# Kernel optimization log

Hardware: AMD Instinct MI355X
Metric: run time of the kernel (lower is better)

The kernel has to match this reference:

```python
import jax, jax.numpy as jnp
import numpy as np

N = 100000; E = 1600000; D_IN = 128; HID = 64; HEADS = 2; OUT = 2; B = 8192
NEG_SLOPE = 0.2


def gat_conv(x, edge_index, W, a_src, a_dst, bias):
    """PyG-style GATConv with add_self_loops=True, concat=False (mean over heads).
    x: [N, Fin], W: [Fin, H*C], a_src/a_dst: [H, C], bias: [C]."""
    n = x.shape[0]
    H, C = a_src.shape
    h = (x @ W).reshape(n, H, C)                      # [N,H,C]
    s_src = (h * a_src[None]).sum(-1)                 # [N,H]
    s_dst = (h * a_dst[None]).sum(-1)                 # [N,H]
    loop = jnp.arange(n, dtype=edge_index.dtype)
    src = jnp.concatenate([edge_index[0], loop])      # [E+N]
    dst = jnp.concatenate([edge_index[1], loop])
    e = jax.nn.leaky_relu(s_src[src] + s_dst[dst], NEG_SLOPE)   # [E+N,H]
    # segment softmax over edges grouped by destination node
    m = jax.ops.segment_max(e, dst, num_segments=n)             # [N,H]
    ex = jnp.exp(e - m[dst])
    z = jax.ops.segment_sum(ex, dst, num_segments=n)            # [N,H]
    alpha = ex / z[dst]                                          # [E+N,H]
    msg = h[src] * alpha[:, :, None]                             # [E+N,H,C]
    out = jax.ops.segment_sum(msg, dst, num_segments=n)         # [N,H,C]
    return out.mean(axis=1) + bias                               # concat=False -> mean over heads


def setup_inputs() -> dict:
    key = jax.random.key(0)
    ks = jax.random.split(key, 32)
    def p(k, shape, fan_in):
        return (jax.random.normal(k, shape, dtype=jnp.float32) / np.sqrt(fan_in)).astype(jnp.float32)
    inp = {}
    inp["x_l"] = jax.random.normal(ks[0], (N, D_IN), dtype=jnp.float32)
    inp["x_r"] = jax.random.normal(ks[1], (N, D_IN), dtype=jnp.float32)
    inp["edge_index_l"] = jax.random.randint(ks[2], (2, E), 0, N, dtype=jnp.int64 if jax.config.jax_enable_x64 else jnp.int32)
    inp["edge_index_r"] = jax.random.randint(ks[3], (2, E), 0, N, dtype=jnp.int64 if jax.config.jax_enable_x64 else jnp.int32)
    inp["labels_l"] = jax.random.randint(ks[4], (B,), 0, N)
    inp["labels_r"] = jax.random.randint(ks[5], (B,), 0, N)
    i = 6
    for side in ("l", "r"):
        inp[f"w1{side}"] = p(ks[i], (D_IN, HEADS * HID), D_IN); i += 1
        inp[f"as1{side}"] = p(ks[i], (HEADS, HID), HID); i += 1
        inp[f"ad1{side}"] = p(ks[i], (HEADS, HID), HID); i += 1
        inp[f"b1{side}"] = jnp.zeros((HID,), jnp.float32)
        inp[f"w2{side}"] = p(ks[i], (HID, HEADS * HID), HID); i += 1
        inp[f"as2{side}"] = p(ks[i], (HEADS, HID), HID); i += 1
        inp[f"ad2{side}"] = p(ks[i], (HEADS, HID), HID); i += 1
        inp[f"b2{side}"] = jnp.zeros((HID,), jnp.float32)
    inp["fc1_w"] = p(ks[i], (2 * HID, HID), 2 * HID); i += 1
    inp["fc1_b"] = jnp.zeros((HID,), jnp.float32)
    inp["fc2_w"] = p(ks[i], (HID, OUT), HID); i += 1
    inp["fc2_b"] = jnp.zeros((OUT,), jnp.float32)
    return inp


def reference(x_l, x_r, edge_index_l, edge_index_r, labels_l, labels_r,
              w1l, as1l, ad1l, b1l, w2l, as2l, ad2l, b2l,
              w1r, as1r, ad1r, b1r, w2r, as2r, ad2r, b2r,
              fc1_w, fc1_b, fc2_w, fc2_b):
    # left tower (dropout is identity in eval mode)
    hl = jax.nn.relu(gat_conv(x_l, edge_index_l, w1l, as1l, ad1l, b1l))
    hl = jax.nn.relu(gat_conv(hl, edge_index_l, w2l, as2l, ad2l, b2l))
    # right tower
    hr = jax.nn.relu(gat_conv(x_r, edge_index_r, w1r, as1r, ad1r, b1r))
    hr = jax.nn.relu(gat_conv(hr, edge_index_r, w2r, as2r, ad2r, b2r))
    # merge_graphs: gather node features per labeled pair, concat
    merged = jnp.concatenate([hl[labels_l], hr[labels_r]], axis=-1)  # [B, 2*HID]
    x = jax.nn.relu(merged @ fc1_w + fc1_b)
    return x @ fc2_w + fc2_b
```

## Files before the change

### kernel.cpp

```cpp
#include <hip/hip_runtime.h>
#include <hip/hip_bf16.h>
#include <hip/hip_fp16.h>

constexpr int NN   = 100000;
constexpr int EE   = 1600000;
constexpr int BB   = 8192;
constexpr int PAD  = 48;
constexpr float NEG_SLOPE = 0.2f;

constexpr int GBM = 128;
constexpr int GB = (NN + GBM - 1) / GBM;
constexpr int AB2 = NN / 8;

constexpr int BSPAN = 256;
constexpr int NB    = (NN + BSPAN - 1) / BSPAN;
constexpr int BCAP  = 5120;
constexpr int CHA   = 4096;
constexpr int NCH   = (EE + CHA - 1) / CHA;

typedef _Float16 f16x8 __attribute__((ext_vector_type(8)));
typedef _Float16 f16x4 __attribute__((ext_vector_type(4)));
typedef float    f32x4 __attribute__((ext_vector_type(4)));

__device__ __forceinline__ float4 ld4(const float* p) { return *(const float4*)p; }

template <typename TIN, int K>
__device__ __forceinline__
void gemm_mfma_body(int bid, const TIN* __restrict__ x,
                    const __half* __restrict__ Wimg,
                    const float* __restrict__ a_src, const float* __restrict__ a_dst,
                    __half* __restrict__ h,
                    float* __restrict__ ssrc, float* __restrict__ sdst,
                    char* lds) {
    constexpr bool HAS_LO = sizeof(TIN) == 4;
    char* const xh = lds;
    char* const xl = HAS_LO ? (lds + 16384) : lds;
    char* const wh = lds + (HAS_LO ? 32768 : 16384);
    char* const wl = wh + 16384;

    const int tid = threadIdx.x;
    const int wid = tid >> 6;
    const int lane = tid & 63;
    const int l15 = lane & 15;
    const int lg = lane >> 4;
    const int row0 = bid * GBM;

    f32x4 acc[2][8];
    #pragma unroll
    for (int i = 0; i < 2; ++i)
        #pragma unroll
        for (int j = 0; j < 8; ++j) acc[i][j] = (f32x4)0.f;

    for (int kt = 0; kt < K; kt += 64) {
        __syncthreads();
        if constexpr (HAS_LO) {
            #pragma unroll
            for (int i = 0; i < 8; ++i) {
                int idx = tid + i * 256;
                int row = idx >> 4, c4 = idx & 15;
                int grow = row0 + row; if (grow >= NN) grow = NN - 1;
                float4 v = ld4(&x[(size_t)grow * K + kt + c4 * 4]);
                f16x4 hv, lv;
                float f0 = v.x; _Float16 h0 = (_Float16)f0; hv[0] = h0; lv[0] = (_Float16)(f0 - (float)h0);
                float f1 = v.y; _Float16 h1 = (_Float16)f1; hv[1] = h1; lv[1] = (_Float16)(f1 - (float)h1);
                float f2 = v.z; _Float16 h2 = (_Float16)f2; hv[2] = h2; lv[2] = (_Float16)(f2 - (float)h2);
                float f3 = v.w; _Float16 h3 = (_Float16)f3; hv[3] = h3; lv[3] = (_Float16)(f3 - (float)h3);
                int byt = row * 128 + ((c4 * 8) ^ ((row & 7) << 4));
                *(f16x4*)(xh + byt) = hv;
                *(f16x4*)(xl + byt) = lv;
            }
        } else {
            #pragma unroll
            for (int i = 0; i < 4; ++i) {
                int idx = tid + i * 256;
                int row = idx >> 3, c8 = idx & 7;
                int grow = row0 + row; if (grow >= NN) grow = NN - 1;
                uint4 v = *(const uint4*)&x[(size_t)grow * 64 + c8 * 8];
                int byt = row * 128 + ((c8 * 16) ^ ((row & 7) << 4));
                *(uint4*)(xh + byt) = v;
            }
        }
        {
            const uint4* ws = (const uint4*)((const char*)Wimg + (size_t)(kt >> 6) * 32768);
            uint4* wd = (uint4*)wh;
            #pragma unroll
            for (int i = 0; i < 8; ++i) wd[tid + i * 256] = ws[tid + i * 256];
        }
        __syncthreads();

        #pragma unroll
        for (int ks = 0; ks < 2; ++ks) {
            const int koff = ks * 64 + lg * 16;
            f16x8 ah[2], al[2];
            #pragma unroll
            for (int rt = 0; rt < 2; ++rt) {
                int row = wid * 32 + rt * 16 + l15;
                int byt = row * 128 + (koff ^ ((row & 7) << 4));
                ah[rt] = *(const f16x8*)(xh + byt);
                if constexpr (HAS_LO) al[rt] = *(const f16x8*)(xl + byt);
            }
            #pragma unroll
            for (int ct = 0; ct < 8; ++ct) {
                int col = ct * 16 + l15;
                int byt = col * 128 + (koff ^ ((col & 7) << 4));
                f16x8 bh = *(const f16x8*)(wh + byt);
                f16x8 bl = *(const f16x8*)(wl + byt);
                #pragma unroll
                for (int rt = 0; rt < 2; ++rt) {
                    acc[rt][ct] = __builtin_amdgcn_mfma_f32_16x16x32_f16(ah[rt], bh, acc[rt][ct], 0, 0, 0);
                    acc[rt][ct] = __builtin_amdgcn_mfma_f32_16x16x32_f16(ah[rt], bl, acc[rt][ct], 0, 0, 0);
                    if constexpr (HAS_LO)
                        acc[rt][ct] = __builtin_amdgcn_mfma_f32_16x16x32_f16(al[rt], bh, acc[rt][ct], 0, 0, 0);
                }
            }
        }
    }

    float sv[8], dv[8];
    #pragma unroll
    for (int ct = 0; ct < 8; ++ct) {
        sv[ct] = a_src[ct * 16 + l15];
        dv[ct] = a_dst[ct * 16 + l15];
    }
    #pragma unroll
    for (int rt = 0; rt < 2; ++rt) {
        #pragma unroll
        for (int r = 0; r < 4; ++r) {
            int row = row0 + wid * 32 + rt * 16 + lg * 4 + r;
            bool ok = row < NN;
            if (ok) {
                #pragma unroll
                for (int ct = 0; ct < 8; ++ct)
                    h[(size_t)row * 128 + ct * 16 + l15] = __float2half(acc[rt][ct][r]);
            }
            float ps0 = 0.f, pd0 = 0.f, ps1 = 0.f, pd1 = 0.f;
            #pragma unroll
            for (int ct = 0; ct < 4; ++ct) {
                ps0 = fmaf(acc[rt][ct][r], sv[ct], ps0);
                pd0 = fmaf(acc[rt][ct][r], dv[ct], pd0);
                ps1 = fmaf(acc[rt][ct + 4][r], sv[ct + 4], ps1);
                pd1 = fmaf(acc[rt][ct + 4][r], dv[ct + 4], pd1);
            }
            ps0 += __shfl_xor(ps0, 1); pd0 += __shfl_xor(pd0, 1);
            ps1 += __shfl_xor(ps1, 1); pd1 += __shfl_xor(pd1, 1);
            ps0 += __shfl_xor(ps0, 2); pd0 += __shfl_xor(pd0, 2);
            ps1 += __shfl_xor(ps1, 2); pd1 += __shfl_xor(pd1, 2);
            ps0 += __shfl_xor(ps0, 4); pd0 += __shfl_xor(pd0, 4);
            ps1 += __shfl_xor(ps1, 4); pd1 += __shfl_xor(pd1, 4);
            ps0 += __shfl_xor(ps0, 8); pd0 += __shfl_xor(pd0, 8);
            ps1 += __shfl_xor(ps1, 8); pd1 += __shfl_xor(pd1, 8);
            if (ok && l15 == 0) {
                ssrc[row * 2 + 0] = ps0;
                ssrc[row * 2 + 1] = ps1;
                sdst[row * 2 + 0] = pd0;
                sdst[row * 2 + 1] = pd1;
            }
        }
    }
}

__global__ __launch_bounds__(256)
void k_bucket(const int* __restrict__ el, const int* __restrict__ er,
              int* __restrict__ buf, int* __restrict__ gcur,
              const float* __restrict__ w1l, const float* __restrict__ w1r,
              const float* __restrict__ w2l, const float* __restrict__ w2r,
              __half* __restrict__ wi1l, __half* __restrict__ wi1r,
              __half* __restrict__ wi2l, __half* __restrict__ wi2r) {
    const int blk0 = blockIdx.x;
    if (blk0 >= 2 * NCH) {
        const int id = blk0 - 2 * NCH;
        const float* W;
        __half* img;
        int kt;
        if (id < 4) {
            W = (id >> 1) ? w1r : w1l;
            img = ((id >> 1) ? wi1r : wi1l) + (size_t)(id & 1) * 16384;
            kt = (id & 1) * 64;
        } else {
            W = (id == 5) ? w2r : w2l;
            img = (id == 5) ? wi2r : wi2l;
            kt = 0;
        }
        _Float16* imgh = (_Float16*)img;
        _Float16* imgl = imgh + 8192;
        for (int i = threadIdx.x; i < 8192; i += 256) {
            int kk = i >> 7, col = i & 127;
            float f = W[(size_t)(kt + kk) * 128 + col];
            _Float16 hi = (_Float16)f;
            _Float16 lo = (_Float16)(f - (float)hi);
            int hidx = col * 64 + (kk ^ ((col & 7) << 3));
            imgh[hidx] = hi;
            imgl[hidx] = lo;
        }
        return;
    }

    __shared__ int2 P0[CHA];
    __shared__ int2 P1[CHA];
    __shared__ int hist[NB];
    __shared__ int st[NB];
    __shared__ int ofs[NB];
    __shared__ int base[NB];
    __shared__ int sc[512];

    const int blk = blk0;
    const bool right = blk >= NCH;
    const int* __restrict__ e = right ? er : el;
    const int sideoff = right ? NB : 0;
    const int cbase = (right ? blk - NCH : blk) * CHA;
    int cnum = EE - cbase; if (cnum > CHA) cnum = CHA;
    const int t = threadIdx.x;

    for (int i = t; i < cnum; i += 256) {
        int2 p; p.x = e[EE + cbase + i]; p.y = e[cbase + i];
        P0[i] = p;
    }
    for (int i = t; i < NB; i += 256) hist[i] = 0;
    __syncthreads();
    for (int i = t; i < cnum; i += 256) atomicAdd(&hist[P0[i].x >> 8], 1);
    __syncthreads();

    sc[t]       = (t < NB)       ? hist[t]       : 0;
    sc[t + 256] = (t + 256 < NB) ? hist[t + 256] : 0;
    __syncthreads();
    for (int off = 1; off < 512; off <<= 1) {
        int a0 = sc[t];
        int a1 = sc[t + 256];
        int b0 = (t >= off)       ? sc[t - off]       : 0;
        int b1 = (t + 256 >= off) ? sc[t + 256 - off] : 0;
        __syncthreads();
        sc[t] = a0 + b0;
        sc[t + 256] = a1 + b1;
        __syncthreads();
    }
    for (int i = t; i < NB; i += 256) {
        int s = sc[i] - hist[i];
        st[i] = s;
        ofs[i] = s;
    }
    __syncthreads();
    for (int i = t; i < cnum; i += 256) {
        int2 p = P0[i];
        int pos = atomicAdd(&ofs[p.x >> 8], 1);
        P1[pos] = p;
    }
    __syncthreads();
    for (int i = t; i < NB; i += 256)
        base[i] = hist[i] ? atomicAdd(&gcur[sideoff + i], hist[i]) : 0;
    __syncthreads();
    for (int j = t; j < cnum; j += 256) {
        int2 p = P1[j];
        int bk = p.x >> 8;
        buf[(size_t)(sideoff + bk) * BCAP + base[bk] + (j - st[bk])] =
            (p.y << 8) | (p.x & 255);
    }
}

__device__ __forceinline__
void csr_body(int blk, const int* __restrict__ buf, const int* __restrict__ gcur,
              int* __restrict__ cntl, int* __restrict__ cntr,
              int* __restrict__ csrl, int* __restrict__ csrr, char* smem) {
    int* lcnt = (int*)smem;
    int* lcsr = (int*)(smem + 1024);

    const bool right = blk >= NB;
    const int bk = right ? blk - NB : blk;
    int* __restrict__ cnt = right ? cntr : cntl;
    int* __restrict__ csr = right ? csrr : csrl;
    const int* __restrict__ src = buf + (size_t)blk * BCAP;
    const int count = gcur[blk];
    const int lo = bk * BSPAN;
    int nn = NN - lo; if (nn > BSPAN) nn = BSPAN;
    const int t = threadIdx.x;

    for (int i = t; i < nn; i += 256) lcnt[i] = 0;
    __syncthreads();
    for (int i = t; i < count; i += 256) {
        int v = src[i];
        int ld = v & 255;
        int s  = (int)((unsigned)v >> 8);
        int slot = atomicAdd(&lcnt[ld], 1);
        lcsr[ld * PAD + slot] = s;
    }
    __syncthreads();
    const int tot4 = (nn * PAD) >> 2;
    int4* __restrict__ dst4 = (int4*)&csr[(size_t)lo * PAD];
    const int4* __restrict__ s4 = (const int4*)lcsr;
    for (int i = t; i < tot4; i += 256) dst4[i] = s4[i];
    for (int i = t; i < nn; i += 256) cnt[lo + i] = lcnt[i];
}

__global__ __launch_bounds__(256)
void k_csr_gemm1(const int* __restrict__ buf, const int* __restrict__ gcur,
                 int* __restrict__ cnt_l, int* __restrict__ cnt_r,
                 int* __restrict__ csr_l, int* __restrict__ csr_r,
                 const float* __restrict__ x_l, const float* __restrict__ x_r,
                 const __half* __restrict__ wi1l, const float* __restrict__ as1l,
                 const float* __restrict__ ad1l,
                 const __half* __restrict__ wi1r, const float* __restrict__ as1r,
                 const float* __restrict__ ad1r,
                 __half* __restrict__ h_l, __half* __restrict__ h_r,
                 float* __restrict__ ssrc_l, float* __restrict__ sdst_l,
                 float* __restrict__ ssrc_r, float* __restrict__ sdst_r) {
    __shared__ __align__(16) char smem[65536];
    int b = blockIdx.x;
    if (b < 2 * NB) {
        csr_body(b, buf, gcur, cnt_l, cnt_r, csr_l, csr_r, smem);
    } else {
        b -= 2 * NB;
        if (b < GB)
            gemm_mfma_body<float, 128>(b, x_l, wi1l, as1l, ad1l,
                                       h_l, ssrc_l, sdst_l, smem);
        else
            gemm_mfma_body<float, 128>(b - GB, x_r, wi1r, as1r, ad1r,
                                       h_r, ssrc_r, sdst_r, smem);
    }
}

__global__ __launch_bounds__(256)
void k_gemm2x(const __half* __restrict__ f_l, const __half* __restrict__ f_r,
              const __half* __restrict__ wi2l, const float* __restrict__ as2l,
              const float* __restrict__ ad2l,
              const __half* __restrict__ wi2r, const float* __restrict__ as2r,
              const float* __restrict__ ad2r,
              __half* __restrict__ h_l, __half* __restrict__ h_r,
              float* __restrict__ ssrc_l, float* __restrict__ sdst_l,
              float* __restrict__ ssrc_r, float* __restrict__ sdst_r) {
    __shared__ __align__(16) char smem[49152];
    int b = blockIdx.x;
    if (b < GB)
        gemm_mfma_body<__half, 64>(b, (const __half*)f_l, wi2l, as2l, ad2l,
                                   h_l, ssrc_l, sdst_l, smem);
    else
        gemm_mfma_body<__half, 64>(b - GB, (const __half*)f_r, wi2r, as2r, ad2r,
                                   h_r, ssrc_r, sdst_r, smem);
}

__device__ __forceinline__
void att_body(int n, const __half* __restrict__ h,
              const float* __restrict__ ssrc, const float* __restrict__ sdst,
              const int* __restrict__ cnt, const int* __restrict__ csr,
              const float* __restrict__ bias, __half* __restrict__ out) {
    const int g  = threadIdx.x & 31;
    const int hs = g >> 4;
    const int j  = g & 15;
    const int ch = g * 4;

    float sd = sdst[n * 2 + hs];
    float es = ssrc[n * 2 + hs] + sd;
    es = es > 0.f ? es : NEG_SLOPE * es;
    const float wself = __expf(es);
    float zl = 0.f;

    uint2 sv = *(const uint2*)&h[(size_t)n * 128 + ch];
    __half2 sh0 = *(__half2*)&sv.x, sh1 = *(__half2*)&sv.y;
    float2 p01 = __half22float2(sh0), p23 = __half22float2(sh1);
    float a0 = wself * p01.x, a1 = wself * p01.y;
    float a2 = wself * p23.x, a3 = wself * p23.y;

    int b = n * PAD;
    const int e = b + cnt[n];
    while (b < e) {
        int c = e - b; if (c > 16) c = 16;
        int idx = b + (j < c ? j : c - 1);
        int sj = csr[idx];
        float ev = ssrc[sj * 2 + hs] + sd;
        ev = ev > 0.f ? ev : NEG_SLOPE * ev;
        float w = (j < c) ? __expf(ev) : 0.f;
        zl += w;
        int jj = 0;
        for (; jj + 4 <= c; jj += 4) {
            int s0 = __shfl(sj, jj,     32);
            int s1 = __shfl(sj, jj + 1, 32);
            int s2 = __shfl(sj, jj + 2, 32);
            int s3 = __shfl(sj, jj + 3, 32);
            float w0 = __shfl(w, hs * 16 + jj,     32);
            float w1 = __shfl(w, hs * 16 + jj + 1, 32);
            float w2 = __shfl(w, hs * 16 + jj + 2, 32);
            float w3 = __shfl(w, hs * 16 + jj + 3, 32);
            uint2 u0 = *(const uint2*)&h[(size_t)(unsigned)(s0 * 128 + ch)];
            uint2 u1 = *(const uint2*)&h[(size_t)(unsigned)(s1 * 128 + ch)];
            uint2 u2 = *(const uint2*)&h[(size_t)(unsigned)(s2 * 128 + ch)];
            uint2 u3 = *(const uint2*)&h[(size_t)(unsigned)(s3 * 128 + ch)];
            float2 f0a = __half22float2(*(__half2*)&u0.x), f0b = __half22float2(*(__half2*)&u0.y);
            float2 f1a = __half22float2(*(__half2*)&u1.x), f1b = __half22float2(*(__half2*)&u1.y);
            float2 f2a = __half22float2(*(__half2*)&u2.x), f2b = __half22float2(*(__half2*)&u2.y);
            float2 f3a = __half22float2(*(__half2*)&u3.x), f3b = __half22float2(*(__half2*)&u3.y);
            a0 = fmaf(w0, f0a.x, a0); a1 = fmaf(w0, f0a.y, a1);
            a2 = fmaf(w0, f0b.x, a2); a3 = fmaf(w0, f0b.y, a3);
            a0 = fmaf(w1, f1a.x, a0); a1 = fmaf(w1, f1a.y, a1);
            a2 = fmaf(w1, f1b.x, a2); a3 = fmaf(w1, f1b.y, a3);
            a0 = fmaf(w2, f2a.x, a0); a1 = fmaf(w2, f2a.y, a1);
            a2 = fmaf(w2, f2b.x, a2); a3 = fmaf(w2, f2b.y, a3);
            a0 = fmaf(w3, f3a.x, a0); a1 = fmaf(w3, f3a.y, a1);
            a2 = fmaf(w3, f3b.x, a2); a3 = fmaf(w3, f3b.y, a3);
        }
        for (; jj < c; ++jj) {
            int s0   = __shfl(sj, jj, 32);
            float w0 = __shfl(w, hs * 16 + jj, 32);
            uint2 u0 = *(const uint2*)&h[(size_t)(unsigned)(s0 * 128 + ch)];
            float2 f0a = __half22float2(*(__half2*)&u0.x), f0b = __half22float2(*(__half2*)&u0.y);
            a0 = fmaf(w0, f0a.x, a0); a1 = fmaf(w0, f0a.y, a1);
            a2 = fmaf(w0, f0b.x, a2); a3 = fmaf(w0, f0b.y, a3);
        }
        b += c;
    }

    zl += __shfl_xor(zl, 1, 32);
    zl += __shfl_xor(zl, 2, 32);
    zl += __shfl_xor(zl, 4, 32);
    zl += __shfl_xor(zl, 8, 32);
    const float z = wself + zl;

    float zi = 1.f / z;
    a0 *= zi; a1 *= zi; a2 *= zi; a3 *= zi;
    a0 = 0.5f * (a0 + __shfl_xor(a0, 16));
    a1 = 0.5f * (a1 + __shfl_xor(a1, 16));
    a2 = 0.5f * (a2 + __shfl_xor(a2, 16));
    a3 = 0.5f * (a3 + __shfl_xor(a3, 16));
    if (hs == 0) {
        float4 bv = *(const float4*)&bias[ch];
        a0 += bv.x; a1 += bv.y; a2 += bv.z; a3 += bv.w;
        a0 = a0 > 0.f ? a0 : 0.f;
        a1 = a1 > 0.f ? a1 : 0.f;
        a2 = a2 > 0.f ? a2 : 0.f;
        a3 = a3 > 0.f ? a3 : 0.f;
        __align__(8) __half2 hp[2];
        hp[0] = __floats2half2_rn(a0, a1);
        hp[1] = __floats2half2_rn(a2, a3);
        *(uint2*)&out[(size_t)n * 64 + ch] = *(uint2*)hp;
    }
}

__global__ __launch_bounds__(256)
void k_att2x(const __half* __restrict__ h_l, const __half* __restrict__ h_r,
             const float* __restrict__ ssrc_l, const float* __restrict__ sdst_l,
             const float* __restrict__ ssrc_r, const float* __restrict__ sdst_r,
             const int* __restrict__ cnt_l, const int* __restrict__ csr_l,
             const int* __restrict__ cnt_r, const int* __restrict__ csr_r,
             const float* __restrict__ bias_l, const float* __restrict__ bias_r,
             __half* __restrict__ feat_l, __half* __restrict__ feat_r) {
    int blk = blockIdx.x;
    bool right = blk >= AB2;
    int n = (blk - (right ? AB2 : 0)) * 8 + (threadIdx.x >> 5);
    if (!right) att_body(n, h_l, ssrc_l, sdst_l, cnt_l, csr_l, bias_l, feat_l);
    else        att_body(n, h_r, ssrc_r, sdst_r, cnt_r, csr_r, bias_r, feat_r);
}

__global__ __launch_bounds__(256)
void k_fc(const __half* __restrict__ fl, const __half* __restrict__ fr,
          const int* __restrict__ ll, const int* __restrict__ lr,
          const float* __restrict__ w1, const float* __restrict__ b1,
          const float* __restrict__ w2, const float* __restrict__ b2,
          float* __restrict__ out) {
    int b = blockIdx.x * 4 + (threadIdx.x >> 6);
    int j = threadIdx.x & 63;
    int la = ll[b], lb = lr[b];
    float v0 = __half2float(fl[(size_t)la * 64 + j]);
    float v1 = __half2float(fr[(size_t)lb * 64 + j]);
    float acc = b1[j];
    #pragma unroll 8
    for (int k = 0; k < 64; ++k)
        acc += __shfl(v0, k, 64) * w1[k * 64 + j];
    #pragma unroll 8
    for (int k = 0; k < 64; ++k)
        acc += __shfl(v1, k, 64) * w1[(64 + k) * 64 + j];
    float x1 = acc > 0.f ? acc : 0.f;
    float p0 = x1 * w2[j * 2 + 0];
    float p1 = x1 * w2[j * 2 + 1];
    #pragma unroll
    for (int o = 32; o >= 1; o >>= 1) {
        p0 += __shfl_xor(p0, o, 64);
        p1 += __shfl_xor(p1, o, 64);
    }
    if (j == 0) {
        out[b * 2 + 0] = p0 + b2[0];
        out[b * 2 + 1] = p1 + b2[1];
    }
}

extern "C" void kernel_launch(void* const* d_in, const int* in_sizes, int n_in,
                              void* d_out, int out_size, void* d_ws, size_t ws_size,
                              hipStream_t stream) {
    const float* x_l  = (const float*)d_in[0];
    const float* x_r  = (const float*)d_in[1];
    const int* ei_l  = (const int*)d_in[2];
    const int* ei_r  = (const int*)d_in[3];
    const int* lab_l = (const int*)d_in[4];
    const int* lab_r = (const int*)d_in[5];
    const float* w1l  = (const float*)d_in[6];
    const float* as1l = (const float*)d_in[7];
    const float* ad1l = (const float*)d_in[8];
    const float* b1l  = (const float*)d_in[9];
    const float* w2l  = (const float*)d_in[10];
    const float* as2l = (const float*)d_in[11];
    const float* ad2l = (const float*)d_in[12];
    const float* b2l  = (const float*)d_in[13];
    const float* w1r  = (const float*)d_in[14];
    const float* as1r = (const float*)d_in[15];
    const float* ad1r = (const float*)d_in[16];
    const float* b1r  = (const float*)d_in[17];
    const float* w2r  = (const float*)d_in[18];
    const float* as2r = (const float*)d_in[19];
    const float* ad2r = (const float*)d_in[20];
    const float* b2r  = (const float*)d_in[21];
    const float* fc1w = (const float*)d_in[22];
    const float* fc1b = (const float*)d_in[23];
    const float* fc2w = (const float*)d_in[24];
    const float* fc2b = (const float*)d_in[25];

    char* p = (char*)d_ws;
    auto alloc = [&](size_t bytes) -> void* {
        void* q = (void*)p;
        p += (bytes + 255) & ~(size_t)255;
        return q;
    };
    __half* h_l    = (__half*)alloc((size_t)NN * 128 * 2);
    __half* h_r    = (__half*)alloc((size_t)NN * 128 * 2);
    __half* feat_l = (__half*)alloc((size_t)NN * 64 * 2);
    __half* feat_r = (__half*)alloc((size_t)NN * 64 * 2);
    float* ssrc_l = (float*)alloc((size_t)NN * 2 * 4);
    float* sdst_l = (float*)alloc((size_t)NN * 2 * 4);
    float* ssrc_r = (float*)alloc((size_t)NN * 2 * 4);
    float* sdst_r = (float*)alloc((size_t)NN * 2 * 4);
    int* cnt2  = (int*)alloc(((size_t)2 * NN + 2 * NB) * 4);
    int* csr_l = (int*)alloc((size_t)NN * PAD * 4);
    int* csr_r = (int*)alloc((size_t)NN * PAD * 4);
    __half* wi1l = (__half*)alloc(65536);
    __half* wi1r = (__half*)alloc(65536);
    __half* wi2l = (__half*)alloc(32768);
    __half* wi2r = (__half*)alloc(32768);
    int* cnt_l = cnt2;
    int* cnt_r = cnt2 + NN;
    int* gcur  = cnt2 + 2 * NN;

    int* buf = (int*)feat_l;

    hipMemsetAsync(gcur, 0, (size_t)2 * NB * 4, stream);

    k_bucket<<<2 * NCH + 6, 256, 0, stream>>>(ei_l, ei_r, buf, gcur,
                                              w1l, w1r, w2l, w2r,
                                              wi1l, wi1r, wi2l, wi2r);

    k_csr_gemm1<<<2 * NB + 2 * GB, 256, 0, stream>>>(
        buf, gcur, cnt_l, cnt_r, csr_l, csr_r,
        x_l, x_r, wi1l, as1l, ad1l, wi1r, as1r, ad1r,
        h_l, h_r, ssrc_l, sdst_l, ssrc_r, sdst_r);

    k_att2x<<<2 * AB2, 256, 0, stream>>>(h_l, h_r, ssrc_l, sdst_l, ssrc_r, sdst_r,
                                         cnt_l, csr_l, cnt_r, csr_r,
                                         b1l, b1r, feat_l, feat_r);

    k_gemm2x<<<2 * GB, 256, 0, stream>>>(feat_l, feat_r,
                                         wi2l, as2l, ad2l, wi2r, as2r, ad2r,
                                         h_l, h_r, ssrc_l, sdst_l, ssrc_r, sdst_r);

    k_att2x<<<2 * AB2, 256, 0, stream>>>(h_l, h_r, ssrc_l, sdst_l, ssrc_r, sdst_r,
                                         cnt_l, csr_l, cnt_r, csr_r,
                                         b2l, b2r, feat_l, feat_r);

    k_fc<<<(BB + 3) / 4, 256, 0, stream>>>(feat_l, feat_r, lab_l, lab_r,
                                           fc1w, fc1b, fc2w, fc2b,
                                           (float*)d_out);
}
```

Baseline: 558.1 us.

## Halve GEMM K-tile and bucket chunk to shrink LDS footprint

```diff
diff --git a/kernel.cpp b/kernel.cpp
--- a/kernel.cpp
+++ b/kernel.cpp
@@ -15,7 +15,7 @@
 constexpr int BSPAN = 256;
 constexpr int NB    = (NN + BSPAN - 1) / BSPAN;
 constexpr int BCAP  = 5120;
-constexpr int CHA   = 4096;
+constexpr int CHA   = 2048;
 constexpr int NCH   = (EE + CHA - 1) / CHA;
 
 typedef _Float16 f16x8 __attribute__((ext_vector_type(8)));
@@ -34,9 +34,9 @@
                     char* lds) {
     constexpr bool HAS_LO = sizeof(TIN) == 4;
     char* const xh = lds;
-    char* const xl = HAS_LO ? (lds + 16384) : lds;
-    char* const wh = lds + (HAS_LO ? 32768 : 16384);
-    char* const wl = wh + 16384;
+    char* const xl = HAS_LO ? (lds + 8192) : lds;
+    char* const wh = lds + (HAS_LO ? 16384 : 8192);
+    char* const wl = wh + 8192;
 
     const int tid = threadIdx.x;
     const int wid = tid >> 6;
@@ -51,13 +51,13 @@
         #pragma unroll
         for (int j = 0; j < 8; ++j) acc[i][j] = (f32x4)0.f;
 
-    for (int kt = 0; kt < K; kt += 64) {
+    for (int kt = 0; kt < K; kt += 32) {
         __syncthreads();
         if constexpr (HAS_LO) {
             #pragma unroll
-            for (int i = 0; i < 8; ++i) {
+            for (int i = 0; i < 4; ++i) {
                 int idx = tid + i * 256;
-                int row = idx >> 4, c4 = idx & 15;
+                int row = idx >> 3, c4 = idx & 7;
                 int grow = row0 + row; if (grow >= NN) grow = NN - 1;
                 float4 v = ld4(&x[(size_t)grow * K + kt + c4 * 4]);
                 f16x4 hv, lv;
@@ -65,53 +65,50 @@
                 float f1 = v.y; _Float16 h1 = (_Float16)f1; hv[1] = h1; lv[1] = (_Float16)(f1 - (float)h1);
                 float f2 = v.z; _Float16 h2 = (_Float16)f2; hv[2] = h2; lv[2] = (_Float16)(f2 - (float)h2);
                 float f3 = v.w; _Float16 h3 = (_Float16)f3; hv[3] = h3; lv[3] = (_Float16)(f3 - (float)h3);
-                int byt = row * 128 + ((c4 * 8) ^ ((row & 7) << 4));
+                int byt = row * 64 + ((c4 * 8) ^ ((row & 3) << 4));
                 *(f16x4*)(xh + byt) = hv;
                 *(f16x4*)(xl + byt) = lv;
             }
         } else {
             #pragma unroll
-            for (int i = 0; i < 4; ++i) {
+            for (int i = 0; i < 2; ++i) {
                 int idx = tid + i * 256;
-                int row = idx >> 3, c8 = idx & 7;
+                int row = idx >> 2, c8 = idx & 3;
                 int grow = row0 + row; if (grow >= NN) grow = NN - 1;
-                uint4 v = *(const uint4*)&x[(size_t)grow * 64 + c8 * 8];
-                int byt = row * 128 + ((c8 * 16) ^ ((row & 7) << 4));
+                uint4 v = *(const uint4*)&x[(size_t)grow * 64 + kt + c8 * 8];
+                int byt = row * 64 + ((c8 * 16) ^ ((row & 3) << 4));
                 *(uint4*)(xh + byt) = v;
             }
         }
         {
-            const uint4* ws = (const uint4*)((const char*)Wimg + (size_t)(kt >> 6) * 32768);
+            const uint4* ws = (const uint4*)((const char*)Wimg + (size_t)(kt >> 5) * 16384);
             uint4* wd = (uint4*)wh;
             #pragma unroll
-            for (int i = 0; i < 8; ++i) wd[tid + i * 256] = ws[tid + i * 256];
+            for (int i = 0; i < 4; ++i) wd[tid + i * 256] = ws[tid + i * 256];
         }
         __syncthreads();
 
+        const int koff = lg * 16;
+        f16x8 ah[2], al[2];
         #pragma unroll
-        for (int ks = 0; ks < 2; ++ks) {
-            const int koff = ks * 64 + lg * 16;
-            f16x8 ah[2], al[2];
+        for (int rt = 0; rt < 2; ++rt) {
+            int row = wid * 32 + rt * 16 + l15;
+            int byt = row * 64 + (koff ^ ((row & 3) << 4));
+            ah[rt] = *(const f16x8*)(xh + byt);
+            if constexpr (HAS_LO) al[rt] = *(const f16x8*)(xl + byt);
+        }
+        #pragma unroll
+        for (int ct = 0; ct < 8; ++ct) {
+            int col = ct * 16 + l15;
+            int byt = col * 64 + (koff ^ ((col & 3) << 4));
+            f16x8 bh = *(const f16x8*)(wh + byt);
+            f16x8 bl = *(const f16x8*)(wl + byt);
             #pragma unroll
             for (int rt = 0; rt < 2; ++rt) {
-                int row = wid * 32 + rt * 16 + l15;
-                int byt = row * 128 + (koff ^ ((row & 7) << 4));
-                ah[rt] = *(const f16x8*)(xh + byt);
-                if constexpr (HAS_LO) al[rt] = *(const f16x8*)(xl + byt);
-            }
-            #pragma unroll
-            for (int ct = 0; ct < 8; ++ct) {
-                int col = ct * 16 + l15;
-                int byt = col * 128 + (koff ^ ((col & 7) << 4));
-                f16x8 bh = *(const f16x8*)(wh + byt);
-                f16x8 bl = *(const f16x8*)(wl + byt);
-                #pragma unroll
-                for (int rt = 0; rt < 2; ++rt) {
-                    acc[rt][ct] = __builtin_amdgcn_mfma_f32_16x16x32_f16(ah[rt], bh, acc[rt][ct], 0, 0, 0);
-                    acc[rt][ct] = __builtin_amdgcn_mfma_f32_16x16x32_f16(ah[rt], bl, acc[rt][ct], 0, 0, 0);
-                    if constexpr (HAS_LO)
-                        acc[rt][ct] = __builtin_amdgcn_mfma_f32_16x16x32_f16(al[rt], bh, acc[rt][ct], 0, 0, 0);
-                }
+                acc[rt][ct] = __builtin_amdgcn_mfma_f32_16x16x32_f16(ah[rt], bh, acc[rt][ct], 0, 0, 0);
+                acc[rt][ct] = __builtin_amdgcn_mfma_f32_16x16x32_f16(ah[rt], bl, acc[rt][ct], 0, 0, 0);
+                if constexpr (HAS_LO)
+                    acc[rt][ct] = __builtin_amdgcn_mfma_f32_16x16x32_f16(al[rt], bh, acc[rt][ct], 0, 0, 0);
             }
         }
     }
@@ -172,31 +169,32 @@
         const float* W;
         __half* img;
         int kt;
-        if (id < 4) {
-            W = (id >> 1) ? w1r : w1l;
-            img = ((id >> 1) ? wi1r : wi1l) + (size_t)(id & 1) * 16384;
-            kt = (id & 1) * 64;
+        if (id < 8) {
+            W = (id >> 2) ? w1r : w1l;
+            img = ((id >> 2) ? wi1r : wi1l) + (size_t)(id & 3) * 8192;
+            kt = (id & 3) * 32;
         } else {
-            W = (id == 5) ? w2r : w2l;
-            img = (id == 5) ? wi2r : wi2l;
-            kt = 0;
+            int jx = id - 8;
+            W = (jx >> 1) ? w2r : w2l;
+            img = ((jx >> 1) ? wi2r : wi2l) + (size_t)(jx & 1) * 8192;
+            kt = (jx & 1) * 32;
         }
         _Float16* imgh = (_Float16*)img;
-        _Float16* imgl = imgh + 8192;
-        for (int i = threadIdx.x; i < 8192; i += 256) {
+        _Float16* imgl = imgh + 4096;
+        for (int i = threadIdx.x; i < 4096; i += 256) {
             int kk = i >> 7, col = i & 127;
             float f = W[(size_t)(kt + kk) * 128 + col];
             _Float16 hi = (_Float16)f;
             _Float16 lo = (_Float16)(f - (float)hi);
-            int hidx = col * 64 + (kk ^ ((col & 7) << 3));
+            int hidx = col * 32 + (kk ^ ((col & 3) << 3));
             imgh[hidx] = hi;
             imgl[hidx] = lo;
         }
         return;
     }
 
-    __shared__ int2 P0[CHA];
-    __shared__ int2 P1[CHA];
+    __shared__ int   P1[CHA];
+    __shared__ short bkof[CHA];
     __shared__ int hist[NB];
     __shared__ int st[NB];
     __shared__ int ofs[NB];
@@ -211,13 +209,12 @@
     int cnum = EE - cbase; if (cnum > CHA) cnum = CHA;
     const int t = threadIdx.x;
 
+    for (int i = t; i < NB; i += 256) hist[i] = 0;
+    __syncthreads();
     for (int i = t; i < cnum; i += 256) {
-        int2 p; p.x = e[EE + cbase + i]; p.y = e[cbase + i];
-        P0[i] = p;
-    }
-    for (int i = t; i < NB; i += 256) hist[i] = 0;
-    __syncthreads();
-    for (int i = t; i < cnum; i += 256) atomicAdd(&hist[P0[i].x >> 8], 1);
+        int d = e[EE + cbase + i];
+        atomicAdd(&hist[d >> 8], 1);
+    }
     __syncthreads();
 
     sc[t]       = (t < NB)       ? hist[t]       : 0;
@@ -240,19 +237,20 @@
     }
     __syncthreads();
     for (int i = t; i < cnum; i += 256) {
-        int2 p = P0[i];
-        int pos = atomicAdd(&ofs[p.x >> 8], 1);
-        P1[pos] = p;
+        int d = e[EE + cbase + i];
+        int s = e[cbase + i];
+        int bk = d >> 8;
+        int pos = atomicAdd(&ofs[bk], 1);
+        P1[pos] = (s << 8) | (d & 255);
+        bkof[pos] = (short)bk;
     }
     __syncthreads();
     for (int i = t; i < NB; i += 256)
         base[i] = hist[i] ? atomicAdd(&gcur[sideoff + i], hist[i]) : 0;
     __syncthreads();
     for (int j = t; j < cnum; j += 256) {
-        int2 p = P1[j];
-        int bk = p.x >> 8;
-        buf[(size_t)(sideoff + bk) * BCAP + base[bk] + (j - st[bk])] =
-            (p.y << 8) | (p.x & 255);
+        int bk = bkof[j];
+        buf[(size_t)(sideoff + bk) * BCAP + base[bk] + (j - st[bk])] = P1[j];
     }
 }
 
@@ -302,7 +300,7 @@
                  __half* __restrict__ h_l, __half* __restrict__ h_r,
                  float* __restrict__ ssrc_l, float* __restrict__ sdst_l,
                  float* __restrict__ ssrc_r, float* __restrict__ sdst_r) {
-    __shared__ __align__(16) char smem[65536];
+    __shared__ __align__(16) char smem[50176];
     int b = blockIdx.x;
     if (b < 2 * NB) {
         csr_body(b, buf, gcur, cnt_l, cnt_r, csr_l, csr_r, smem);
@@ -326,7 +324,7 @@
               __half* __restrict__ h_l, __half* __restrict__ h_r,
               float* __restrict__ ssrc_l, float* __restrict__ sdst_l,
               float* __restrict__ ssrc_r, float* __restrict__ sdst_r) {
-    __shared__ __align__(16) char smem[49152];
+    __shared__ __align__(16) char smem[24576];
     int b = blockIdx.x;
     if (b < GB)
         gemm_mfma_body<__half, 64>(b, (const __half*)f_l, wi2l, as2l, ad2l,
@@ -538,9 +536,9 @@
 
     hipMemsetAsync(gcur, 0, (size_t)2 * NB * 4, stream);
 
-    k_bucket<<<2 * NCH + 6, 256, 0, stream>>>(ei_l, ei_r, buf, gcur,
-                                              w1l, w1r, w2l, w2r,
-                                              wi1l, wi1r, wi2l, wi2r);
+    k_bucket<<<2 * NCH + 12, 256, 0, stream>>>(ei_l, ei_r, buf, gcur,
+                                               w1l, w1r, w2l, w2r,
+                                               wi1l, wi1r, wi2l, wi2r);
 
     k_csr_gemm1<<<2 * NB + 2 * GB, 256, 0, stream>>>(
         buf, gcur, cnt_l, cnt_r, csr_l, csr_r,
```

Result: faster. 546.8 us (-2.0%).
